# Performance work log

Measured on AMD Instinct MI355X. Metric: run time of the kernel, lower is better.

## Reference

```python
import jax, jax.numpy as jnp
import numpy as np

B = 100000  # number of index rows
R1, N1, N2, N3, R2 = 1, 200, 200, 50, 32


def setup_inputs() -> dict:
    key = jax.random.key(0)
    k0, k1, k2, k3, k4 = jax.random.split(key, 5)
    TT_core = jax.random.normal(k0, (R1, N1, N2, N3, R2), dtype=jnp.float32)
    # Kernel (gram) matrices per mode, as produced by e.g. an RBF kernel on
    # side information; positive entries in [0,1) like an RBF gram matrix.
    K1 = jax.random.uniform(k1, (N1, N1), dtype=jnp.float32)
    K2 = jax.random.uniform(k2, (N2, N2), dtype=jnp.float32)
    K3 = jax.random.uniform(k3, (N3, N3), dtype=jnp.float32)
    # Multi-index: one column per tensor mode; kept in [0, 50) so it is
    # in-range for every mode (N3 = 50 is the smallest).
    indices = jax.random.randint(k4, (B, 3), 0, N3, dtype=jnp.int64)
    return {"TT_core": TT_core, "K1": K1, "K2": K2, "K3": K3, "indices": indices}


def reference(TT_core, K1, K2, K3, indices):
    # lazy_mode_product(T, K, mode) == contract K over the given tensor mode.
    # TT_core axes: (r1, i, j, k, r2)
    T = jnp.einsum('ai,rijks->rajks', K1, TT_core)   # mode 1
    T = jnp.einsum('bj,rajks->rabks', K2, T)         # mode 2
    T = jnp.einsum('ck,rabks->rabcs', K3, T)         # mode 3
    # Auxiliary regularization term (full_grad=False branch of TT_kernel_component)
    reg = T * TT_core
    # T.permute([1,2,3,0,-1])[i1,i2,i3] -> (B, r1, r2) multi-index gather
    Tp = jnp.transpose(T, (1, 2, 3, 0, 4))           # (n1, n2, n3, r1, r2)
    out = Tp[indices[:, 0], indices[:, 1], indices[:, 2]]  # (B, r1, r2)
    return out, reg
```

## Files before the change

### kernel.cpp

```cpp
#include <hip/hip_runtime.h>
#include <type_traits>


typedef float    f32x4 __attribute__((ext_vector_type(4)));
typedef _Float16 half8 __attribute__((ext_vector_type(8)));
typedef unsigned short ushort8 __attribute__((ext_vector_type(8)));
typedef unsigned short u16;
typedef unsigned int   u32;

#define N12   200
#define N3    50
#define R2    32
#define SJK   320000
#define SKS   1600
#define NTOT  64000000
#define OUT_ELEMS 3200000
#define APAD  208
#define KPAD  224
#define BROW  136
#define K3B_HALVES 4096

__global__ __launch_bounds__(256) void k_prep(
    const float* __restrict__ K1, const float* __restrict__ K2,
    const float* __restrict__ K3, u16* __restrict__ kh) {
  int t = blockIdx.x * 256 + threadIdx.x;
  const int total = APAD * KPAD;
  if (t >= 2 * total + K3B_HALVES) return;
  float x;
  if (t < 2 * total) {
    const float* src = (t < total) ? K1 : K2;
    int tt = (t < total) ? t : t - total;
    int r = tt / KPAD, c = tt % KPAD;
    x = (r < N12 && c < N12) ? src[r * N12 + c] : 0.f;
  } else {
    int u = t - 2 * total;
    int e = u & 7, l = (u >> 3) & 63, frag = u >> 9;
    int c = (frag & 3) * 16 + (l & 15);
    int k = (frag >> 2) * 32 + (l >> 4) * 8 + e;
    x = (c < N3 && k < N3) ? K3[c * N3 + k] : 0.f;
  }
  kh[t] = __builtin_bit_cast(u16, (_Float16)x);
}

template <typename BT>
__global__ __launch_bounds__(512, 4) void k_gemm(
    const BT* __restrict__ Bsrc, const u16* __restrict__ Ah,
    u16* __restrict__ Dout) {
  constexpr bool BF32 = std::is_same_v<BT, float>;
  __shared__ __align__(16) u16 As[2][APAD * 32];
  __shared__ __align__(16) u16 Bl[2][32 * BROW];
  const int tid  = threadIdx.x;
  const int lane = tid & 63;
  const int wave = tid >> 6;
  const int l15  = lane & 15;
  const int kg   = lane >> 4;
  const int orig = blockIdx.x;
  const int xcd = orig & 7, pos = orig >> 3;
  const int blk = (xcd < 4 ? xcd * 313 : 4 * 313 + (xcd - 4) * 312) + pos;
  const int nblk = blk * 128;
  const int n0   = nblk + wave * 16 + l15;

  const int arow0 = tid >> 2,  ac4 = tid & 3;
  const int arow1 = (tid + 512) >> 2, ac4b = tid & 3;
  const bool a1v  = tid < 320;
  const int brow  = tid >> 4,  bc8 = tid & 15;

  int4 ra0, ra1;
  f32x4 rb0, rb1;
  ushort8 rbh;

#define GLOAD(S)                                                              \
  { ra0 = *(const int4*)(Ah + arow0 * KPAD + (S) * 32 + ac4 * 8);             \
    if (a1v) ra1 = *(const int4*)(Ah + arow1 * KPAD + (S) * 32 + ac4b * 8);   \
    int r = (S) * 32 + brow; if (r > 199) r = 199;                            \
    if constexpr (BF32) {                                                     \
      const float* bp = (const float*)Bsrc + (long)r * SJK + nblk + bc8 * 8;  \
      rb0 = *(const f32x4*)bp; rb1 = *(const f32x4*)(bp + 4);                 \
    } else {                                                                  \
      rbh = *(const ushort8*)((const u16*)Bsrc + (long)r * SJK + nblk + bc8 * 8); \
    } }

#define DSWRITE(BUF)                                                          \
  { *(int4*)(&As[BUF][arow0 * 32 + ac4 * 8]) = ra0;                           \
    if (a1v) *(int4*)(&As[BUF][arow1 * 32 + ac4b * 8]) = ra1;                 \
    if constexpr (BF32) {                                                     \
      ushort8 h;                                                              \
      _Pragma("unroll")                                                       \
      for (int e = 0; e < 4; ++e) {                                           \
        h[e]     = __builtin_bit_cast(u16, (_Float16)rb0[e]);                 \
        h[e + 4] = __builtin_bit_cast(u16, (_Float16)rb1[e]);                 \
      }                                                                       \
      *(ushort8*)(&Bl[BUF][brow * BROW + bc8 * 8]) = h;                       \
    } else {                                                                  \
      *(ushort8*)(&Bl[BUF][brow * BROW + bc8 * 8]) = rbh;                     \
    } }

#define COMPUTE(BUF)                                                          \
  { half8 bh;                                                                 \
    _Pragma("unroll")                                                         \
    for (int e = 0; e < 8; ++e)                                               \
      bh[e] = __builtin_bit_cast(_Float16,                                    \
                  Bl[BUF][(kg * 8 + e) * BROW + wave * 16 + l15]);            \
    _Pragma("unroll")                                                         \
    for (int t = 0; t < 13; ++t) {                                            \
      half8 ah = *(const half8*)(&As[BUF][(t * 16 + l15) * 32 + kg * 8]);     \
      acc[t] = __builtin_amdgcn_mfma_f32_16x16x32_f16(ah, bh, acc[t], 0,0,0); \
    } }

  f32x4 acc[13];
#pragma unroll
  for (int t = 0; t < 13; ++t)
#pragma unroll
    for (int q = 0; q < 4; ++q) acc[t][q] = 0.f;

  GLOAD(0)
  DSWRITE(0)
  __syncthreads();
#pragma unroll
  for (int s = 0; s < 7; ++s) {
    if (s < 6) GLOAD(s + 1)
    COMPUTE(s & 1)
    __syncthreads();
    if (s < 6) {
      DSWRITE((s + 1) & 1)
      __syncthreads();
    }
  }

  const int j  = (u32)n0 / 1600u;
  const int m2 = n0 - j * 1600;
  u16* dbase = Dout + (long)j * SJK + m2;
#pragma unroll
  for (int t = 0; t < 13; ++t) {
    const int rb = t * 16 + kg * 4;
#pragma unroll
    for (int r = 0; r < 4; ++r) {
      const int row = rb + r;
      if (row < N12)
        dbase[(long)row * SKS] = __builtin_bit_cast(u16, (_Float16)acc[t][r]);
    }
  }
#undef GLOAD
#undef DSWRITE
#undef COMPUTE
}

__global__ __launch_bounds__(256, 4) void k_contract_k_mfma(
    const u16* __restrict__ T2h, const float* __restrict__ TT,
    const u16* __restrict__ K3B, float* __restrict__ reg) {
  __shared__ __align__(16) u16 bs[K3B_HALVES];
  __shared__ __align__(16) u16 sl[4][32 * 64];
  const int tid  = threadIdx.x;
  {
    const int4* src = (const int4*)K3B;
    int4* dst = (int4*)bs;
    dst[tid] = src[tid];
    dst[tid + 256] = src[tid + 256];
  }
  const int lane = tid & 63;
  const int wave = tid >> 6;
  const int l15  = lane & 15;
  const int kg   = lane >> 4;
  const int ab   = blockIdx.x * 4 + wave;
  const int base = ab * SKS;
  u16* s_ = &sl[wave][0];

  {
    ushort8 z;
#pragma unroll
    for (int e = 0; e < 8; ++e) z[e] = 0;
#pragma unroll
    for (int c = 0; c < 4; ++c)
      *(ushort8*)(&s_[(c * 64 + lane) * 8]) = z;
  }
#pragma unroll
  for (int c = 0; c < 4; ++c) {
    const int ch = c * 64 + lane;
    if (ch < 200) {
      ushort8 v = *(const ushort8*)(T2h + base + ch * 8);
      const int k  = ch >> 2;
      const int s0 = (ch & 3) * 8;
#pragma unroll
      for (int j = 0; j < 8; ++j)
        s_[(s0 + j) * 64 + (k ^ (j << 3))] = v[j];
    }
  }
  __syncthreads();

  half8 bf[2][4];
#pragma unroll
  for (int ks = 0; ks < 2; ++ks)
#pragma unroll
    for (int cs = 0; cs < 4; ++cs)
      bf[ks][cs] = *(const half8*)(bs + ((ks * 4 + cs) * 64 + lane) * 8);

  half8 af[2][2];
#pragma unroll
  for (int rt = 0; rt < 2; ++rt)
#pragma unroll
    for (int ks = 0; ks < 2; ++ks) {
      const int s = rt * 16 + l15;
      af[rt][ks] = *(const half8*)(
          &s_[s * 64 + ((ks * 32 + kg * 8) ^ ((s & 7) << 3))]);
    }

  f32x4 acc[2][4];
#pragma unroll
  for (int rt = 0; rt < 2; ++rt)
#pragma unroll
    for (int cs = 0; cs < 4; ++cs)
#pragma unroll
      for (int q = 0; q < 4; ++q) acc[rt][cs][q] = 0.f;

#pragma unroll
  for (int rt = 0; rt < 2; ++rt)
#pragma unroll
    for (int ks = 0; ks < 2; ++ks)
#pragma unroll
      for (int cs = 0; cs < 4; ++cs)
        acc[rt][cs] = __builtin_amdgcn_mfma_f32_16x16x32_f16(
            af[rt][ks], bf[ks][cs], acc[rt][cs], 0, 0, 0);

#pragma unroll
  for (int cs = 0; cs < 4; ++cs) {
    const int c = cs * 16 + l15;
    if (c < N3) {
      const int o0 = base + c * R2 + kg * 4;
      f32x4 tv0 = *(const f32x4*)(TT + o0);
      f32x4 tv1 = *(const f32x4*)(TT + o0 + 16);
      f32x4 r0, r1;
#pragma unroll
      for (int q = 0; q < 4; ++q) {
        r0[q] = acc[0][cs][q] * tv0[q];
        r1[q] = acc[1][cs][q] * tv1[q];
      }
      *(f32x4*)(reg + o0) = r0;
      *(f32x4*)(reg + o0 + 16) = r1;
    }
  }
}

template <typename T>
__global__ __launch_bounds__(256) void k_gather(
    const T* T2, const float* __restrict__ K3,
    const int* __restrict__ idx, float* __restrict__ out) {
  int g = blockIdx.x * 256 + threadIdx.x;
  int n = g >> 5, s = g & 31;
  int a = idx[n * 3 + 0], b = idx[n * 3 + 1], c = idx[n * 3 + 2];
  const T* t2 = T2 + a * SJK + b * SKS + s;
  const float* k3r = K3 + c * N3;
  float acc = 0.f;
#pragma unroll
  for (int k = 0; k < N3; ++k) {
    float v;
    if constexpr (std::is_same_v<T, float>) v = t2[k * R2];
    else v = (float)__builtin_bit_cast(_Float16, t2[k * R2]);
    acc = fmaf(k3r[k], v, acc);
  }
  out[g] = acc;
}

__global__ __launch_bounds__(256) void k_transpose(
    const float* __restrict__ K2, float* __restrict__ K2T) {
  int t = blockIdx.x * 256 + threadIdx.x;
  if (t < N12 * N12) {
    int i = t / N12, a = t % N12;
    K2T[t] = K2[a * N12 + i];
  }
}

__global__ __launch_bounds__(256) void k_fallback_ci(
    const float* __restrict__ TT, const float* __restrict__ K1T,
    float* __restrict__ T1) {
  const int m  = blockIdx.x * 256 + threadIdx.x;
  const int a0 = blockIdx.y * 50;
  float acc[50];
#pragma unroll
  for (int aa = 0; aa < 50; ++aa) acc[aa] = 0.f;
#pragma unroll 2
  for (int i = 0; i < N12; ++i) {
    float v = TT[i * SJK + m];
    const float* kr = K1T + i * N12 + a0;
#pragma unroll
    for (int aa = 0; aa < 50; ++aa) acc[aa] = fmaf(kr[aa], v, acc[aa]);
  }
#pragma unroll
  for (int aa = 0; aa < 50; ++aa) T1[(a0 + aa) * SJK + m] = acc[aa];
}

__global__ __launch_bounds__(256) void k_contract_j_inplace(
    float* T12, const float* __restrict__ K2T) {
  __shared__ float lds[N12 * 80];
  const int a    = blockIdx.y;
  const int m0   = blockIdx.x * 80;
  const int base = a * SJK + m0;
  for (int t = threadIdx.x; t < N12 * 80; t += 256) {
    int j = t / 80, ml = t % 80;
    lds[t] = T12[base + j * SKS + ml];
  }
  __syncthreads();
  for (int o = threadIdx.x; o < N12 * 80; o += 256) {
    int b = o / 80, ml = o % 80;
    float acc = 0.f;
#pragma unroll 4
    for (int j = 0; j < N12; ++j)
      acc = fmaf(K2T[j * N12 + b], lds[j * 80 + ml], acc);
    T12[base + b * SKS + ml] = acc;
  }
}

__global__ __launch_bounds__(256) void k_contract_k_reg(
    const float* T2, const float* __restrict__ TT,
    const float* __restrict__ K3, float* reg) {
  const int t  = blockIdx.x * 256 + threadIdx.x;
  const int s  = t & 31;
  const int ab = t >> 5;
  const int base = ab * SKS + s;
  float v[N3];
#pragma unroll
  for (int k = 0; k < N3; ++k) v[k] = T2[base + k * R2];
  for (int c = 0; c < N3; ++c) {
    const float* k3r = K3 + c * N3;
    float a0 = 0.f, a1 = 0.f, a2 = 0.f, a3 = 0.f;
#pragma unroll
    for (int k = 0; k < 48; k += 4) {
      a0 = fmaf(k3r[k],     v[k],     a0);
      a1 = fmaf(k3r[k + 1], v[k + 1], a1);
      a2 = fmaf(k3r[k + 2], v[k + 2], a2);
      a3 = fmaf(k3r[k + 3], v[k + 3], a3);
    }
    a0 = fmaf(k3r[48], v[48], a0);
    a1 = fmaf(k3r[49], v[49], a1);
    const int o = base + c * R2;
    reg[o] = ((a0 + a1) + (a2 + a3)) * TT[o];
  }
}

extern "C" void kernel_launch(void* const* d_in, const int* in_sizes, int n_in,
                              void* d_out, int out_size, void* d_ws, size_t ws_size,
                              hipStream_t stream) {
  const float* TT  = (const float*)d_in[0];
  const float* K1  = (const float*)d_in[1];
  const float* K2  = (const float*)d_in[2];
  const float* K3  = (const float*)d_in[3];
  const int*   idx = (const int*)d_in[4];

  float* out = (float*)d_out;
  float* reg = out + OUT_ELEMS;
  u16* kh = (u16*)d_out;
  const int matoff = APAD * KPAD;
  const u16* k3b = kh + 2 * matoff;

  k_prep<<<dim3((2 * matoff + K3B_HALVES + 255) / 256), 256, 0, stream>>>(
      K1, K2, K3, kh);

  const size_t need = (size_t)NTOT * sizeof(u16);
  if (ws_size >= need) {
    u16* T1h = (u16*)reg;
    u16* T2h = (u16*)d_ws;
    k_gemm<float><<<dim3(2500), 512, 0, stream>>>(TT, kh, T1h);
    k_gemm<u16><<<dim3(2500), 512, 0, stream>>>(T1h, kh + matoff, T2h);
    k_contract_k_mfma<<<dim3(40000 / 4), 256, 0, stream>>>(T2h, TT, k3b, reg);
    k_gather<u16><<<dim3(OUT_ELEMS / 256), 256, 0, stream>>>(T2h, K3, idx, out);
  } else {
    float* k1t = out;
    float* k2t = out + N12 * N12;
    k_transpose<<<dim3((N12 * N12 + 255) / 256), 256, 0, stream>>>(K1, k1t);
    k_transpose<<<dim3((N12 * N12 + 255) / 256), 256, 0, stream>>>(K2, k2t);
    k_fallback_ci<<<dim3(SJK / 256, 4), 256, 0, stream>>>(TT, k1t, reg);
    k_contract_j_inplace<<<dim3(20, N12), 256, 0, stream>>>(reg, k2t);
    k_gather<float><<<dim3(OUT_ELEMS / 256), 256, 0, stream>>>(reg, K3, idx, out);
    k_contract_k_reg<<<dim3(40000 * 32 / 256), 256, 0, stream>>>(reg, TT, K3, reg);
  }
}
```

Measured before the change: 342.5 us.

## Drop redundant GEMM barrier, raise contract occupancy, vectorize gather by two

Removes the extra __syncthreads after each MFMA compute stage in the double-buffered GEMM, relying on the barrier after the LDS write to order buffer reuse. Raises the minimum waves-per-EU hint for the K3 contraction kernel from 4 to 6, which may force register limits. Rewrites the half-precision gather so each thread loads two adjacent fp16 values and writes a float2, halving the thread count. The fp32 fallback gather is split out as its own kernel.

```diff
diff --git a/kernel.cpp b/kernel.cpp
--- a/kernel.cpp
+++ b/kernel.cpp
@@ -120,7 +120,6 @@
   for (int s = 0; s < 7; ++s) {
     if (s < 6) GLOAD(s + 1)
     COMPUTE(s & 1)
-    __syncthreads();
     if (s < 6) {
       DSWRITE((s + 1) & 1)
       __syncthreads();
@@ -145,7 +144,7 @@
 #undef COMPUTE
 }
 
-__global__ __launch_bounds__(256, 4) void k_contract_k_mfma(
+__global__ __launch_bounds__(256, 6) void k_contract_k_mfma(
     const u16* __restrict__ T2h, const float* __restrict__ TT,
     const u16* __restrict__ K3B, float* __restrict__ reg) {
   __shared__ __align__(16) u16 bs[K3B_HALVES];
@@ -240,24 +239,22 @@
   }
 }
 
-template <typename T>
-__global__ __launch_bounds__(256) void k_gather(
-    const T* T2, const float* __restrict__ K3,
+__global__ __launch_bounds__(256) void k_gather2(
+    const u16* __restrict__ T2h, const float* __restrict__ K3,
     const int* __restrict__ idx, float* __restrict__ out) {
   int g = blockIdx.x * 256 + threadIdx.x;
-  int n = g >> 5, s = g & 31;
+  int n = g >> 4, sp = (g & 15) * 2;
   int a = idx[n * 3 + 0], b = idx[n * 3 + 1], c = idx[n * 3 + 2];
-  const T* t2 = T2 + a * SJK + b * SKS + s;
+  const u16* t2 = T2h + a * SJK + b * SKS + sp;
   const float* k3r = K3 + c * N3;
-  float acc = 0.f;
+  float acc0 = 0.f, acc1 = 0.f;
 #pragma unroll
   for (int k = 0; k < N3; ++k) {
-    float v;
-    if constexpr (std::is_same_v<T, float>) v = t2[k * R2];
-    else v = (float)__builtin_bit_cast(_Float16, t2[k * R2]);
-    acc = fmaf(k3r[k], v, acc);
-  }
-  out[g] = acc;
+    ushort2 v = *(const ushort2*)(t2 + k * R2);
+    acc0 = fmaf(k3r[k], (float)__builtin_bit_cast(_Float16, v.x), acc0);
+    acc1 = fmaf(k3r[k], (float)__builtin_bit_cast(_Float16, v.y), acc1);
+  }
+  *(float2*)(out + n * R2 + sp) = make_float2(acc0, acc1);
 }
 
 __global__ __launch_bounds__(256) void k_transpose(
@@ -309,6 +306,20 @@
   }
 }
 
+__global__ __launch_bounds__(256) void k_gather_f32(
+    const float* T2, const float* __restrict__ K3,
+    const int* __restrict__ idx, float* __restrict__ out) {
+  int g = blockIdx.x * 256 + threadIdx.x;
+  int n = g >> 5, s = g & 31;
+  int a = idx[n * 3 + 0], b = idx[n * 3 + 1], c = idx[n * 3 + 2];
+  const float* t2 = T2 + a * SJK + b * SKS + s;
+  const float* k3r = K3 + c * N3;
+  float acc = 0.f;
+#pragma unroll
+  for (int k = 0; k < N3; ++k) acc = fmaf(k3r[k], t2[k * R2], acc);
+  out[g] = acc;
+}
+
 __global__ __launch_bounds__(256) void k_contract_k_reg(
     const float* T2, const float* __restrict__ TT,
     const float* __restrict__ K3, float* reg) {
@@ -361,7 +372,7 @@
     k_gemm<float><<<dim3(2500), 512, 0, stream>>>(TT, kh, T1h);
     k_gemm<u16><<<dim3(2500), 512, 0, stream>>>(T1h, kh + matoff, T2h);
     k_contract_k_mfma<<<dim3(40000 / 4), 256, 0, stream>>>(T2h, TT, k3b, reg);
-    k_gather<u16><<<dim3(OUT_ELEMS / 256), 256, 0, stream>>>(T2h, K3, idx, out);
+    k_gather2<<<dim3(OUT_ELEMS / 512), 256, 0, stream>>>(T2h, K3, idx, out);
   } else {
     float* k1t = out;
     float* k2t = out + N12 * N12;
@@ -369,7 +380,7 @@
     k_transpose<<<dim3((N12 * N12 + 255) / 256), 256, 0, stream>>>(K2, k2t);
     k_fallback_ci<<<dim3(SJK / 256, 4), 256, 0, stream>>>(TT, k1t, reg);
     k_contract_j_inplace<<<dim3(20, N12), 256, 0, stream>>>(reg, k2t);
-    k_gather<float><<<dim3(OUT_ELEMS / 256), 256, 0, stream>>>(reg, K3, idx, out);
+    k_gather_f32<<<dim3(OUT_ELEMS / 256), 256, 0, stream>>>(reg, K3, idx, out);
     k_contract_k_reg<<<dim3(40000 * 32 / 256), 256, 0, stream>>>(reg, TT, K3, reg);
   }
 }
```

Measured after the change: 339.7 us. Within noise of the previous version (-0.8%).
